# Optimization experiments

Hardware: AMD Instinct MI355X
Metric: run time of the kernel (lower is better)

## Reference

```python
import jax, jax.numpy as jnp
import numpy as np

B, S, D, H = 2, 2048, 1024, 16
DH = D // H
DIM_K = 1024


def setup_inputs() -> dict:
    key = jax.random.key(0)
    ks = jax.random.split(key, 5)
    sc = 0.02
    return {
        "x": jax.random.normal(ks[0], (B, S, D), dtype=jnp.float32),
        "Wq": jax.random.normal(ks[1], (D, DIM_K), dtype=jnp.float32) * sc,
        "Wk": jax.random.normal(ks[2], (D, DIM_K), dtype=jnp.float32) * sc,
        "Wv": jax.random.normal(ks[3], (D, DIM_K), dtype=jnp.float32) * sc,
        "Wo": jax.random.normal(ks[4], (DIM_K, DIM_K), dtype=jnp.float32) * sc,
    }


def reference(x, Wq, Wk, Wv, Wo):
    # projections (Linear, no bias); weights stored as [in, out]
    q = (x @ Wq).reshape(B, S, H, DH).transpose(0, 2, 1, 3)  # [B,H,S,DH]
    k = (x @ Wk).reshape(B, S, H, DH).transpose(0, 2, 1, 3)
    v = (x @ Wv).reshape(B, S, H, DH).transpose(0, 2, 1, 3)

    scores = jnp.einsum("bhqd,bhkd->bhqk", q, k)  # [B,H,S,S]
    # causal mask applied BEFORE scaling, as in the original
    causal_mask = jnp.triu(jnp.ones((S, S), dtype=bool), k=1)
    m_inf = -jnp.finfo(scores.dtype).max
    scores = jnp.where(causal_mask[None, None], m_inf, scores)
    attn = jax.nn.softmax(scores * (DIM_K ** -0.5), axis=-1)

    out = jnp.einsum("bhqk,bhkd->bhqd", attn, v)  # [B,H,S,DH]
    out = out.transpose(0, 2, 1, 3).reshape(B, S, DIM_K)
    return out @ Wo
```

## Files before the change

### kernel.cpp

```cpp
#include <hip/hip_runtime.h>


#define AS1 __attribute__((address_space(1)))
#define AS3 __attribute__((address_space(3)))
#define EXPC2 0.04508422f
#define C24 1.08202128f

typedef __attribute__((ext_vector_type(4))) float f32x4;
typedef __attribute__((ext_vector_type(8))) short bf16x8;

__device__ __forceinline__ void gload16(const void* g, void* l) {
  __builtin_amdgcn_global_load_lds((const AS1 unsigned int*)g,
                                   (AS3 unsigned int*)l, 16, 0, 0);
}
__device__ __forceinline__ unsigned short f2b(float f) {
  unsigned u = __float_as_uint(f);
  return (unsigned short)((u + 0x7FFFu + ((u >> 16) & 1u)) >> 16);
}
__device__ __forceinline__ float fexp2(float x) {
  float r;
  asm("v_exp_f32 %0, %1" : "=v"(r) : "v"(x));
  return r;
}
__device__ __forceinline__ unsigned cvtpk(float a, float b) {
  unsigned r;
  asm("v_cvt_pk_bf16_f32 %0, %1, %2" : "=v"(r) : "v"(a), "v"(b));
  return r;
}

__global__ __launch_bounds__(256) void prep(
    const float* __restrict__ x, const float* __restrict__ W0,
    const float* __restrict__ W1, const float* __restrict__ W2,
    const float* __restrict__ W3, unsigned short* __restrict__ xb,
    unsigned short* __restrict__ Wt) {
  __shared__ float T[64][65];
  const int tid = threadIdx.x;
  const int bid = blockIdx.x;
  if (bid < 4096) {
    const size_t i = (size_t)(bid * 256 + tid) * 4;
    float4 v = *(const float4*)&x[i];
    uint2 o;
    o.x = f2b(v.x) | ((unsigned)f2b(v.y) << 16);
    o.y = f2b(v.z) | ((unsigned)f2b(v.w) << 16);
    *(uint2*)&xb[i] = o;
    return;
  }
  const int idx = bid - 4096;
  const int kb = (idx & 15) * 64, nb = ((idx >> 4) & 15) * 64, z = idx >> 8;
  const float* W = (z == 0) ? W0 : (z == 1) ? W1 : (z == 2) ? W2 : W3;
  unsigned short* D = Wt + (size_t)z * 1024 * 1024;
#pragma unroll
  for (int p = 0; p < 4; ++p) {
    const int s = p * 256 + tid;
    const int r = s >> 4, c4 = s & 15;
    float4 v = *(const float4*)&W[(size_t)(kb + r) * 1024 + nb + c4 * 4];
    T[r][c4 * 4 + 0] = v.x;
    T[r][c4 * 4 + 1] = v.y;
    T[r][c4 * 4 + 2] = v.z;
    T[r][c4 * 4 + 3] = v.w;
  }
  __syncthreads();
#pragma unroll
  for (int p = 0; p < 4; ++p) {
    const int s = p * 256 + tid;
    const int n = s >> 4, k4 = s & 15;
    uint2 o;
    o.x = f2b(T[k4 * 4 + 0][n]) | ((unsigned)f2b(T[k4 * 4 + 1][n]) << 16);
    o.y = f2b(T[k4 * 4 + 2][n]) | ((unsigned)f2b(T[k4 * 4 + 3][n]) << 16);
    *(uint2*)&D[(size_t)(nb + n) * 1024 + kb + k4 * 4] = o;
  }
}

__global__ __launch_bounds__(512, 2) void gemm_qkv(
    const unsigned short* __restrict__ xb, const unsigned short* __restrict__ Wt,
    unsigned short* __restrict__ Qb, unsigned short* __restrict__ Kb,
    unsigned short* __restrict__ Vp) {
  __shared__ unsigned short smem[65536];

  const int tid = threadIdx.x, lane = tid & 63, w = tid >> 6;
  const int bm = blockIdx.x & 15, bn = blockIdx.x >> 4;
  const int wr = w >> 2, wc = w & 3;

  f32x4 acc[8][4];
#pragma unroll
  for (int m = 0; m < 8; ++m)
#pragma unroll
    for (int n = 0; n < 4; ++n) acc[m][n] = (f32x4)0.0f;

  const int prow0 = tid >> 3, pc0 = tid & 7;
  const int u0 = pc0 ^ (prow0 & 7);
  const int aRow0 = bm * 256 + 2 * prow0 + (u0 >> 2);
  const int bRow0 = bn * 256 + 2 * prow0 + (u0 >> 2);
  const int cOff = (u0 & 3) * 8;

  const int fr = lane & 15, g = lane >> 4;
  const int frh = fr >> 1;
  const int pcx = ((((fr & 1) << 2) | g) ^ frh) * 8;

#define STAGE8(BUF, KS, KC)                                                   \
  {                                                                           \
    const size_t ko = (size_t)(KC) + (KS)*32 + cOff;                          \
    gload16(&xb[(size_t)aRow0 * 1024 + ko],                                   \
            &smem[(BUF)*32768 + (KS)*8192 + tid * 8]);                        \
    gload16(&xb[(size_t)(aRow0 + 128) * 1024 + ko],                           \
            &smem[(BUF)*32768 + (KS)*8192 + 4096 + tid * 8]);                 \
    gload16(&Wt[(size_t)bRow0 * 1024 + ko],                                   \
            &smem[(BUF)*32768 + 16384 + (KS)*8192 + tid * 8]);                \
    gload16(&Wt[(size_t)(bRow0 + 128) * 1024 + ko],                           \
            &smem[(BUF)*32768 + 16384 + (KS)*8192 + 4096 + tid * 8]);         \
  }

#define PHASE(CUR, KS, VMSTR, STAGESTMT)                                      \
  {                                                                           \
    asm volatile(VMSTR ::: "memory");                                         \
    __builtin_amdgcn_sched_barrier(0);                                        \
    __builtin_amdgcn_s_barrier();                                             \
    __builtin_amdgcn_sched_barrier(0);                                        \
    bf16x8 af[8], bf[4];                                                      \
    const unsigned short* Ab_ = &smem[(CUR)*32768 + (KS)*8192];               \
    const unsigned short* Bb_ = &smem[(CUR)*32768 + 16384 + (KS)*8192];       \
    _Pragma("unroll") for (int mf = 0; mf < 8; ++mf) af[mf] =                 \
        *(const bf16x8*)&Ab_[(wr * 64 + mf * 8 + frh) * 64 + pcx];            \
    _Pragma("unroll") for (int nf = 0; nf < 4; ++nf) bf[nf] =                 \
        *(const bf16x8*)&Bb_[(wc * 32 + nf * 8 + frh) * 64 + pcx];            \
    STAGESTMT;                                                                \
    __builtin_amdgcn_s_setprio(1);                                            \
    _Pragma("unroll") for (int mf = 0; mf < 8; ++mf)                          \
        _Pragma("unroll") for (int nf = 0; nf < 4; ++nf) acc[mf][nf] =        \
            __builtin_amdgcn_mfma_f32_16x16x32_bf16(af[mf], bf[nf],           \
                                                    acc[mf][nf], 0, 0, 0);    \
    __builtin_amdgcn_s_setprio(0);                                            \
  }

  STAGE8(0, 0, 0)
  STAGE8(0, 1, 0)

#pragma unroll 1
  for (int t = 0; t < 15; ++t) {
    const int cu_ = t & 1, nb_ = (t + 1) & 1;
    const int kc1 = (t + 1) * 64;
    PHASE(cu_, 0, "s_waitcnt vmcnt(4)", STAGE8(nb_, 0, kc1))
    PHASE(cu_, 1, "s_waitcnt vmcnt(4)", STAGE8(nb_, 1, kc1))
  }
  PHASE(1, 0, "s_waitcnt vmcnt(4)", (void)0)
  PHASE(1, 1, "s_waitcnt vmcnt(0)", (void)0)

  if (bn < 8) {
    unsigned short* Ob = (bn < 4) ? Qb : Kb;
    const int cbase = (bn & 3) * 256;
#pragma unroll
    for (int mf = 0; mf < 8; ++mf)
#pragma unroll
      for (int nf = 0; nf < 4; ++nf) {
        const int col = cbase + wc * 64 + nf * 16 + fr;
        const int h = col >> 6, d = col & 63;
#pragma unroll
        for (int rr = 0; rr < 4; ++rr) {
          const int m = bm * 256 + wr * 128 + mf * 16 + g * 4 + rr;
          const int b = m >> 11, s = m & 2047;
          Ob[((size_t)(b * 16 + h) * 2048 + s) * 64 + d] = f2b(acc[mf][nf][rr]);
        }
      }
    return;
  }

  const int chb = (bn - 8) * 256;
  const int s0all = bm * 256;
  const int b = s0all >> 11;
#pragma unroll
  for (int qq = 0; qq < 4; ++qq) {
    const int qm = qq >> 1, qn = qq & 1;
    __syncthreads();
    if (wr == qm && (wc >> 1) == qn) {
#pragma unroll
      for (int mf = 0; mf < 8; ++mf)
#pragma unroll
        for (int nf = 0; nf < 4; ++nf) {
          const int cl = (wc & 1) * 64 + nf * 16 + fr;
#pragma unroll
          for (int rr = 0; rr < 4; ++rr) {
            const int ml = mf * 16 + g * 4 + rr;
            const int u = ml & 63, a = u >> 4;
            const int sperm = (ml & 64) | ((a >> 1) * 32 + ((u >> 2) & 3) * 8 +
                                           (a & 1) * 4 + (u & 3));
            smem[cl * 132 + sperm] = f2b(acc[mf][nf][rr]);
          }
        }
    }
    __syncthreads();
    const int row = tid >> 2, cg = (tid & 3) * 32;
    const int ch = chb + qn * 128 + row;
    const int h = ch >> 6, d = ch & 63;
    const int sb = (s0all + qm * 128) & 2047;
    unsigned short* dst = &Vp[((size_t)(b * 16 + h) * 64 + d) * 2048 + sb + cg];
    *(uint4*)(dst + 0) = *(const uint4*)&smem[row * 132 + cg];
    *(uint4*)(dst + 8) = *(const uint4*)&smem[row * 132 + cg + 8];
    *(uint4*)(dst + 16) = *(const uint4*)&smem[row * 132 + cg + 16];
    *(uint4*)(dst + 24) = *(const uint4*)&smem[row * 132 + cg + 24];
  }
#undef PHASE
#undef STAGE8
}

__global__ __launch_bounds__(256) void gemm_out(
    const unsigned short* __restrict__ A, const unsigned short* __restrict__ B,
    float* __restrict__ Of) {
  __shared__ unsigned short smem[32768];

  const int tid = threadIdx.x, lane = tid & 63, w = tid >> 6;
  const int bm = blockIdx.x >> 3, bn = blockIdx.x & 7;
  const int wr = w >> 1, wc = w & 1;

  f32x4 acc[4][4];
#pragma unroll
  for (int m = 0; m < 4; ++m)
#pragma unroll
    for (int n = 0; n < 4; ++n) acc[m][n] = (f32x4)0.0f;

  const int prow0 = tid >> 3, pc0 = tid & 7;
  const int u0 = pc0 ^ (prow0 & 7);
  const int rOff = 2 * prow0 + (u0 >> 2);
  const int cOff = (u0 & 3) * 8;

  const int fr = lane & 15, g = lane >> 4;
  const int frh = fr >> 1;
  const int pcx = ((((fr & 1) << 2) | g) ^ frh) * 8;

#define OSTAGE4(BUF, KS, KC)                                                  \
  {                                                                           \
    const size_t ko = (size_t)(KC) + (KS)*32 + cOff;                          \
    gload16(&A[(size_t)(bm * 128 + rOff) * 1024 + ko],                        \
            &smem[(BUF)*16384 + (KS)*4096 + tid * 8]);                        \
    gload16(&A[(size_t)(bm * 128 + 64 + rOff) * 1024 + ko],                   \
            &smem[(BUF)*16384 + (KS)*4096 + 2048 + tid * 8]);                 \
    gload16(&B[(size_t)(bn * 128 + rOff) * 1024 + ko],                        \
            &smem[(BUF)*16384 + 8192 + (KS)*4096 + tid * 8]);                 \
    gload16(&B[(size_t)(bn * 128 + 64 + rOff) * 1024 + ko],                   \
            &smem[(BUF)*16384 + 8192 + (KS)*4096 + 2048 + tid * 8]);          \
  }

#define OPHASE(CUR, KS, VMSTR, STAGESTMT)                                     \
  {                                                                           \
    asm volatile(VMSTR ::: "memory");                                         \
    __builtin_amdgcn_sched_barrier(0);                                        \
    __builtin_amdgcn_s_barrier();                                             \
    __builtin_amdgcn_sched_barrier(0);                                        \
    bf16x8 af[4], bf[4];                                                      \
    const unsigned short* Ab_ = &smem[(CUR)*16384 + (KS)*4096];               \
    const unsigned short* Bb_ = &smem[(CUR)*16384 + 8192 + (KS)*4096];        \
    _Pragma("unroll") for (int mf = 0; mf < 4; ++mf) af[mf] =                 \
        *(const bf16x8*)&Ab_[(wr * 32 + mf * 8 + frh) * 64 + pcx];            \
    _Pragma("unroll") for (int nf = 0; nf < 4; ++nf) bf[nf] =                 \
        *(const bf16x8*)&Bb_[(wc * 32 + nf * 8 + frh) * 64 + pcx];            \
    STAGESTMT;                                                                \
    __builtin_amdgcn_s_setprio(1);                                            \
    _Pragma("unroll") for (int mf = 0; mf < 4; ++mf)                          \
        _Pragma("unroll") for (int nf = 0; nf < 4; ++nf) acc[mf][nf] =        \
            __builtin_amdgcn_mfma_f32_16x16x32_bf16(af[mf], bf[nf],           \
                                                    acc[mf][nf], 0, 0, 0);    \
    __builtin_amdgcn_s_setprio(0);                                            \
  }

  OSTAGE4(0, 0, 0)
  OSTAGE4(0, 1, 0)

#pragma unroll 1
  for (int t = 0; t < 15; ++t) {
    const int cu_ = t & 1, nb_ = (t + 1) & 1;
    const int kc1 = (t + 1) * 64;
    OPHASE(cu_, 0, "s_waitcnt vmcnt(4)", OSTAGE4(nb_, 0, kc1))
    OPHASE(cu_, 1, "s_waitcnt vmcnt(4)", OSTAGE4(nb_, 1, kc1))
  }
  OPHASE(1, 0, "s_waitcnt vmcnt(4)", (void)0)
  OPHASE(1, 1, "s_waitcnt vmcnt(0)", (void)0)

#pragma unroll
  for (int mf = 0; mf < 4; ++mf)
#pragma unroll
    for (int nf = 0; nf < 4; ++nf) {
      const int col = bn * 128 + wc * 64 + nf * 16 + fr;
#pragma unroll
      for (int rr = 0; rr < 4; ++rr) {
        const int m = bm * 128 + wr * 64 + mf * 16 + g * 4 + rr;
        Of[(size_t)m * 1024 + col] = acc[mf][nf][rr];
      }
    }
#undef OPHASE
#undef OSTAGE4
}

__global__ __launch_bounds__(256) void attn_fm(
    const unsigned short* __restrict__ Qb, const unsigned short* __restrict__ Kb,
    const unsigned short* __restrict__ Vp, unsigned short* __restrict__ Ab) {
  __shared__ unsigned short smem[16384];

  const int tid = threadIdx.x, lane = tid & 63, w = tid >> 6;
  const int lo = lane & 15, hi = lane >> 4;

  const int id = blockIdx.x;
  const int qtr = id >> 8;
  const int g = (id >> 5) & 7;
  const int bh = id & 31;
  const int bq = (qtr == 0)   ? 2 * g
                 : (qtr == 1) ? 2 * g + 1
                 : (qtr == 2) ? 31 - 2 * g
                              : 30 - 2 * g;
  const int qw = bq * 64 + w * 16;
  const size_t base = (size_t)bh * (2048 * 64);

  bf16x8 qf[2];
#pragma unroll
  for (int ks = 0; ks < 2; ++ks)
    qf[ks] =
        *(const bf16x8*)&Qb[base + (size_t)(qw + lo) * 64 + ks * 32 + hi * 8];

  f32x4 accO[4];
#pragma unroll
  for (int mf = 0; mf < 4; ++mf) accO[mf] = (f32x4)0.0f;
  float lpart = 0.0f;

  const int ntile = bq + 1;
  const unsigned short* kgb = Kb + base;
  const unsigned short* vgb = Vp + base;
  const int lseg = w * 512;

#define STAGE(BUF, KBASE)                                                    \
  {                                                                          \
    const int kb_ = (KBASE);                                                 \
    _Pragma("unroll") for (int qq = 0; qq < 2; ++qq) {                       \
      const int slot = qq * 256 + tid;                                       \
      const int row = slot >> 3, ch = (slot & 7) ^ (row & 7);                \
      gload16(kgb + (size_t)(kb_ + row) * 64 + ch * 8,                       \
              &smem[(BUF)*4096 + qq * 2048 + lseg]);                         \
      gload16(vgb + (size_t)row * 2048 + kb_ + ch * 8,                       \
              &smem[8192 + (BUF)*4096 + qq * 2048 + lseg]);                  \
    }                                                                        \
  }

  STAGE(0, 0)
  int cur = 0;

  for (int t = 0; t < ntile; ++t) {
    __syncthreads();
    if (t + 1 < ntile) STAGE(cur ^ 1, (t + 1) * 64)

    const int kb = t * 64;
    const int x7 = lo & 7;
    bf16x8 ka[2][4];
#pragma unroll
    for (int ks = 0; ks < 2; ++ks) {
      const int ch = (ks * 4 + hi) ^ x7;
#pragma unroll
      for (int kf = 0; kf < 4; ++kf)
        ka[ks][kf] =
            *(const bf16x8*)&smem[cur * 4096 + (kf * 16 + lo) * 64 + ch * 8];
    }
    f32x4 st[4];
#pragma unroll
    for (int kf = 0; kf < 4; ++kf) st[kf] = (f32x4)0.0f;
    __builtin_amdgcn_s_setprio(1);
#pragma unroll
    for (int ks = 0; ks < 2; ++ks)
#pragma unroll
      for (int kf = 0; kf < 4; ++kf)
        st[kf] = __builtin_amdgcn_mfma_f32_16x16x32_bf16(ka[ks][kf], qf[ks],
                                                         st[kf], 0, 0, 0);
    __builtin_amdgcn_s_setprio(0);

    bf16x8 va[2][4];
#pragma unroll
    for (int ks = 0; ks < 2; ++ks) {
      const int ch = (ks * 4 + hi) ^ x7;
#pragma unroll
      for (int mf = 0; mf < 4; ++mf)
        va[ks][mf] = *(const bf16x8*)&smem[8192 + cur * 4096 +
                                           (mf * 16 + lo) * 64 + ch * 8];
    }

    float v[16];
#pragma unroll
    for (int kf = 0; kf < 4; ++kf)
#pragma unroll
      for (int rr = 0; rr < 4; ++rr) v[kf * 4 + rr] = st[kf][rr];
    if (kb + 63 > qw) {
      const int qg = qw + lo;
#pragma unroll
      for (int kf = 0; kf < 4; ++kf)
#pragma unroll
        for (int rr = 0; rr < 4; ++rr)
          if (kb + kf * 16 + hi * 4 + rr > qg) v[kf * 4 + rr] = -1e30f;
    }
    float p[16], rs = 0.0f;
#pragma unroll
    for (int i = 0; i < 16; ++i) {
      p[i] = fexp2(fmaf(v[i], EXPC2, -C24));
      rs += p[i];
    }
    lpart += rs;

    bf16x8 pb[2];
#pragma unroll
    for (int ks = 0; ks < 2; ++ks) {
      uint4 u;
      u.x = cvtpk(p[ks * 8 + 0], p[ks * 8 + 1]);
      u.y = cvtpk(p[ks * 8 + 2], p[ks * 8 + 3]);
      u.z = cvtpk(p[ks * 8 + 4], p[ks * 8 + 5]);
      u.w = cvtpk(p[ks * 8 + 6], p[ks * 8 + 7]);
      pb[ks] = *(bf16x8*)&u;
    }

    __builtin_amdgcn_s_setprio(1);
#pragma unroll
    for (int ks = 0; ks < 2; ++ks)
#pragma unroll
      for (int mf = 0; mf < 4; ++mf)
        accO[mf] = __builtin_amdgcn_mfma_f32_16x16x32_bf16(va[ks][mf], pb[ks],
                                                           accO[mf], 0, 0, 0);
    __builtin_amdgcn_s_setprio(0);
    cur ^= 1;
  }

  __syncthreads();

  float l = lpart;
  l += __shfl_xor(l, 16);
  l += __shfl_xor(l, 32);
  const float linv = 1.0f / l;
  unsigned short* ot = &smem[w * 1152];
#pragma unroll
  for (int mf = 0; mf < 4; ++mf) {
    uint2 u;
    u.x = cvtpk(accO[mf][0] * linv, accO[mf][1] * linv);
    u.y = cvtpk(accO[mf][2] * linv, accO[mf][3] * linv);
    *(uint2*)&ot[lo * 72 + mf * 16 + hi * 4] = u;
  }
  const int b = bh >> 4, h = bh & 15;
  const int row = lane >> 2, cg = (lane & 3) * 16;
  uint4 o0 = *(const uint4*)&ot[row * 72 + cg];
  uint4 o1 = *(const uint4*)&ot[row * 72 + cg + 8];
  unsigned short* op = &Ab[(size_t)(b * 2048 + qw + row) * 1024 + h * 64 + cg];
  *(uint4*)op = o0;
  *(uint4*)(op + 8) = o1;
#undef STAGE
}

extern "C" void kernel_launch(void* const* d_in, const int* in_sizes, int n_in,
                              void* d_out, int out_size, void* d_ws,
                              size_t ws_size, hipStream_t stream) {
  (void)in_sizes; (void)n_in; (void)out_size; (void)ws_size;
  const float* x = (const float*)d_in[0];
  const float* Wq = (const float*)d_in[1];
  const float* Wk = (const float*)d_in[2];
  const float* Wv = (const float*)d_in[3];
  const float* Wo = (const float*)d_in[4];
  float* out = (float*)d_out;

  char* ws = (char*)d_ws;
  unsigned short* xb = (unsigned short*)(ws);
  unsigned short* Wt = (unsigned short*)(ws + (8u << 20));
  unsigned short* Qb = (unsigned short*)(ws + (16u << 20));
  unsigned short* Kb = (unsigned short*)(ws + (24u << 20));
  unsigned short* Vp = (unsigned short*)(ws + (32u << 20));
  unsigned short* Ab = (unsigned short*)(ws + (40u << 20));
  unsigned short* Wto = Wt + (size_t)3 * 1024 * 1024;

  prep<<<dim3(5120), 256, 0, stream>>>(x, Wq, Wk, Wv, Wo, xb, Wt);
  gemm_qkv<<<dim3(192), 512, 0, stream>>>(xb, Wt, Qb, Kb, Vp);
  attn_fm<<<dim3(1024), 256, 0, stream>>>(Qb, Kb, Vp, Ab);
  gemm_out<<<dim3(256), 256, 0, stream>>>(Ab, Wto, out);
}
```

Before: 94.44 us.

## Pair causal query blocks per workgroup with triple-buffered K/V pipeline

The attention kernel now gives each workgroup two query blocks, p and 31-p, so every workgroup processes a fixed 33 key tiles. This balances the causal workload and halves the grid to 512 blocks. K/V staging moves from double to triple buffering, with explicit vmcnt waits and raw s_barrier phases that separate the K and V loads. LDS use rises to about 58KB per block, which may reduce occupancy, and the fixed vmcnt counts depend on exactly how the loads are issued.

```diff
diff --git a/kernel.cpp b/kernel.cpp
--- a/kernel.cpp
+++ b/kernel.cpp
@@ -289,159 +289,179 @@
 #undef OSTAGE4
 }
 
-__global__ __launch_bounds__(256) void attn_fm(
+__global__ __launch_bounds__(256) void attn_pipe(
     const unsigned short* __restrict__ Qb, const unsigned short* __restrict__ Kb,
     const unsigned short* __restrict__ Vp, unsigned short* __restrict__ Ab) {
-  __shared__ unsigned short smem[16384];
+  __shared__ unsigned short smem[29184];
 
   const int tid = threadIdx.x, lane = tid & 63, w = tid >> 6;
   const int lo = lane & 15, hi = lane >> 4;
+  const int x7 = lo & 7;
 
   const int id = blockIdx.x;
-  const int qtr = id >> 8;
-  const int g = (id >> 5) & 7;
   const int bh = id & 31;
-  const int bq = (qtr == 0)   ? 2 * g
-                 : (qtr == 1) ? 2 * g + 1
-                 : (qtr == 2) ? 31 - 2 * g
-                              : 30 - 2 * g;
-  const int qw = bq * 64 + w * 16;
+  const int p = id >> 5;
+  const int qw0 = p * 64 + w * 16;
+  const int qw1 = (31 - p) * 64 + w * 16;
   const size_t base = (size_t)bh * (2048 * 64);
-
-  bf16x8 qf[2];
-#pragma unroll
-  for (int ks = 0; ks < 2; ++ks)
-    qf[ks] =
-        *(const bf16x8*)&Qb[base + (size_t)(qw + lo) * 64 + ks * 32 + hi * 8];
-
-  f32x4 accO[4];
-#pragma unroll
-  for (int mf = 0; mf < 4; ++mf) accO[mf] = (f32x4)0.0f;
-  float lpart = 0.0f;
-
-  const int ntile = bq + 1;
   const unsigned short* kgb = Kb + base;
   const unsigned short* vgb = Vp + base;
   const int lseg = w * 512;
-
-#define STAGE(BUF, KBASE)                                                    \
+  const int b = bh >> 4, h = bh & 15;
+
+  auto kbof = [&](int s) { return (s <= p ? s : s - p - 1) * 64; };
+
+  bf16x8 qA0, qA1, qB0, qB1;
+  qA0 = *(const bf16x8*)&Qb[base + (size_t)(qw0 + lo) * 64 + 0 * 32 + hi * 8];
+  qA1 = *(const bf16x8*)&Qb[base + (size_t)(qw0 + lo) * 64 + 1 * 32 + hi * 8];
+  qB0 = *(const bf16x8*)&Qb[base + (size_t)(qw1 + lo) * 64 + 0 * 32 + hi * 8];
+  qB1 = *(const bf16x8*)&Qb[base + (size_t)(qw1 + lo) * 64 + 1 * 32 + hi * 8];
+  bf16x8 qc0 = qA0, qc1 = qA1;
+
+  f32x4 accO[4];
+#pragma unroll
+  for (int mf = 0; mf < 4; ++mf) accO[mf] = (f32x4)0.0f;
+  float lpart = 0.0f;
+  int qwc = qw0;
+
+  const int srow = tid >> 3;
+  const int sch = ((tid & 7) ^ (srow & 7)) * 8;
+
+#define AST(BUF, KB_)                                                        \
   {                                                                          \
-    const int kb_ = (KBASE);                                                 \
-    _Pragma("unroll") for (int qq = 0; qq < 2; ++qq) {                       \
-      const int slot = qq * 256 + tid;                                       \
-      const int row = slot >> 3, ch = (slot & 7) ^ (row & 7);                \
-      gload16(kgb + (size_t)(kb_ + row) * 64 + ch * 8,                       \
-              &smem[(BUF)*4096 + qq * 2048 + lseg]);                         \
-      gload16(vgb + (size_t)row * 2048 + kb_ + ch * 8,                       \
-              &smem[8192 + (BUF)*4096 + qq * 2048 + lseg]);                  \
+    const int kb_ = (KB_);                                                   \
+    gload16(kgb + (size_t)(kb_ + srow) * 64 + sch, &smem[(BUF)*4096 + lseg]); \
+    gload16(kgb + (size_t)(kb_ + 32 + srow) * 64 + sch,                      \
+            &smem[(BUF)*4096 + 2048 + lseg]);                                \
+    __builtin_amdgcn_sched_barrier(0);                                       \
+    gload16(vgb + (size_t)srow * 2048 + kb_ + sch,                           \
+            &smem[12288 + (BUF)*4096 + lseg]);                               \
+    gload16(vgb + (size_t)(32 + srow) * 2048 + kb_ + sch,                    \
+            &smem[12288 + (BUF)*4096 + 2048 + lseg]);                        \
+    __builtin_amdgcn_sched_barrier(0);                                       \
+  }
+
+#define KPHASE(CB, VMSTR)                                                    \
+  asm volatile(VMSTR ::: "memory");                                          \
+  __builtin_amdgcn_sched_barrier(0);                                         \
+  __builtin_amdgcn_s_barrier();                                              \
+  __builtin_amdgcn_sched_barrier(0);                                         \
+  bf16x8 ka[2][4];                                                           \
+  _Pragma("unroll") for (int ks = 0; ks < 2; ++ks) {                         \
+    const int ch = (ks * 4 + hi) ^ x7;                                       \
+    _Pragma("unroll") for (int kf = 0; kf < 4; ++kf) ka[ks][kf] =            \
+        *(const bf16x8*)&smem[(CB)*4096 + (kf * 16 + lo) * 64 + ch * 8];     \
+  }                                                                          \
+  f32x4 st[4];                                                               \
+  _Pragma("unroll") for (int kf = 0; kf < 4; ++kf) st[kf] = (f32x4)0.0f;     \
+  __builtin_amdgcn_s_setprio(1);                                             \
+  _Pragma("unroll") for (int ks = 0; ks < 2; ++ks) {                         \
+    _Pragma("unroll") for (int kf = 0; kf < 4; ++kf) st[kf] =                \
+        __builtin_amdgcn_mfma_f32_16x16x32_bf16(                             \
+            ka[ks][kf], (ks == 0) ? qc0 : qc1, st[kf], 0, 0, 0);             \
+  }                                                                          \
+  __builtin_amdgcn_s_setprio(0);
+
+#define VPHASE(CB, VMSTR, STAGESTMT, KBV)                                    \
+  asm volatile(VMSTR ::: "memory");                                          \
+  __builtin_amdgcn_sched_barrier(0);                                         \
+  __builtin_amdgcn_s_barrier();                                              \
+  __builtin_amdgcn_sched_barrier(0);                                         \
+  bf16x8 va[2][4];                                                           \
+  _Pragma("unroll") for (int ks = 0; ks < 2; ++ks) {                         \
+    const int ch = (ks * 4 + hi) ^ x7;                                       \
+    _Pragma("unroll") for (int mf = 0; mf < 4; ++mf) va[ks][mf] =            \
+        *(const bf16x8*)&smem[12288 + (CB)*4096 + (mf * 16 + lo) * 64 +      \
+                              ch * 8];                                       \
+  }                                                                          \
+  STAGESTMT;                                                                 \
+  float v[16];                                                               \
+  _Pragma("unroll") for (int kf = 0; kf < 4; ++kf)                           \
+      _Pragma("unroll") for (int rr = 0; rr < 4; ++rr) v[kf * 4 + rr] =      \
+          st[kf][rr];                                                        \
+  if ((KBV) + 63 > qwc) {                                                    \
+    const int qg = qwc + lo;                                                 \
+    _Pragma("unroll") for (int kf = 0; kf < 4; ++kf)                         \
+        _Pragma("unroll") for (int rr = 0; rr < 4; ++rr) if ((KBV) +         \
+            kf * 16 + hi * 4 + rr > qg) v[kf * 4 + rr] = -1e30f;             \
+  }                                                                          \
+  float pe[16], rs = 0.0f;                                                   \
+  _Pragma("unroll") for (int i = 0; i < 16; ++i) {                           \
+    pe[i] = fexp2(fmaf(v[i], EXPC2, -C24));                                  \
+    rs += pe[i];                                                             \
+  }                                                                          \
+  lpart += rs;                                                               \
+  bf16x8 pb[2];                                                              \
+  _Pragma("unroll") for (int ks = 0; ks < 2; ++ks) {                         \
+    uint4 u;                                                                 \
+    u.x = cvtpk(pe[ks * 8 + 0], pe[ks * 8 + 1]);                             \
+    u.y = cvtpk(pe[ks * 8 + 2], pe[ks * 8 + 3]);                             \
+    u.z = cvtpk(pe[ks * 8 + 4], pe[ks * 8 + 5]);                             \
+    u.w = cvtpk(pe[ks * 8 + 6], pe[ks * 8 + 7]);                             \
+    pb[ks] = *(bf16x8*)&u;                                                   \
+  }                                                                          \
+  __builtin_amdgcn_s_setprio(1);                                             \
+  _Pragma("unroll") for (int ks = 0; ks < 2; ++ks)                           \
+      _Pragma("unroll") for (int mf = 0; mf < 4; ++mf) accO[mf] =            \
+          __builtin_amdgcn_mfma_f32_16x16x32_bf16(va[ks][mf], pb[ks],        \
+                                                  accO[mf], 0, 0, 0);        \
+  __builtin_amdgcn_s_setprio(0);
+
+#define EPI(QW)                                                              \
+  {                                                                          \
+    float l = lpart;                                                         \
+    l += __shfl_xor(l, 16);                                                  \
+    l += __shfl_xor(l, 32);                                                  \
+    const float linv = 1.0f / l;                                             \
+    unsigned short* ot = &smem[24576 + w * 1152];                            \
+    _Pragma("unroll") for (int mf = 0; mf < 4; ++mf) {                       \
+      uint2 u;                                                               \
+      u.x = cvtpk(accO[mf][0] * linv, accO[mf][1] * linv);                   \
+      u.y = cvtpk(accO[mf][2] * linv, accO[mf][3] * linv);                   \
+      *(uint2*)&ot[lo * 72 + mf * 16 + hi * 4] = u;                          \
     }                                                                        \
-  }
-
-  STAGE(0, 0)
-  int cur = 0;
-
-  for (int t = 0; t < ntile; ++t) {
-    __syncthreads();
-    if (t + 1 < ntile) STAGE(cur ^ 1, (t + 1) * 64)
-
-    const int kb = t * 64;
-    const int x7 = lo & 7;
-    bf16x8 ka[2][4];
-#pragma unroll
-    for (int ks = 0; ks < 2; ++ks) {
-      const int ch = (ks * 4 + hi) ^ x7;
-#pragma unroll
-      for (int kf = 0; kf < 4; ++kf)
-        ka[ks][kf] =
-            *(const bf16x8*)&smem[cur * 4096 + (kf * 16 + lo) * 64 + ch * 8];
+    const int row_ = lane >> 2, cg_ = (lane & 3) * 16;                       \
+    uint4 o0 = *(const uint4*)&ot[row_ * 72 + cg_];                          \
+    uint4 o1 = *(const uint4*)&ot[row_ * 72 + cg_ + 8];                      \
+    unsigned short* op =                                                     \
+        &Ab[(size_t)(b * 2048 + (QW) + row_) * 1024 + h * 64 + cg_];         \
+    *(uint4*)op = o0;                                                        \
+    *(uint4*)(op + 8) = o1;                                                  \
+  }
+
+  AST(0, 0)
+  AST(1, kbof(1))
+
+#pragma unroll 1
+  for (int c = 0; c < 32; ++c) {
+    const int cb = c % 3;
+    const int kb = kbof(c);
+    {
+      KPHASE(cb, "s_waitcnt vmcnt(6)")
+      VPHASE(cb, "s_waitcnt vmcnt(4)",
+             if (c < 31) AST((c + 2) % 3, kbof(c + 2)), kb)
     }
-    f32x4 st[4];
-#pragma unroll
-    for (int kf = 0; kf < 4; ++kf) st[kf] = (f32x4)0.0f;
-    __builtin_amdgcn_s_setprio(1);
-#pragma unroll
-    for (int ks = 0; ks < 2; ++ks)
-#pragma unroll
-      for (int kf = 0; kf < 4; ++kf)
-        st[kf] = __builtin_amdgcn_mfma_f32_16x16x32_bf16(ka[ks][kf], qf[ks],
-                                                         st[kf], 0, 0, 0);
-    __builtin_amdgcn_s_setprio(0);
-
-    bf16x8 va[2][4];
-#pragma unroll
-    for (int ks = 0; ks < 2; ++ks) {
-      const int ch = (ks * 4 + hi) ^ x7;
-#pragma unroll
-      for (int mf = 0; mf < 4; ++mf)
-        va[ks][mf] = *(const bf16x8*)&smem[8192 + cur * 4096 +
-                                           (mf * 16 + lo) * 64 + ch * 8];
+    if (c == p) {
+      EPI(qw0)
+#pragma unroll
+      for (int mf = 0; mf < 4; ++mf) accO[mf] = (f32x4)0.0f;
+      lpart = 0.0f;
+      qc0 = qB0;
+      qc1 = qB1;
+      qwc = qw1;
     }
-
-    float v[16];
-#pragma unroll
-    for (int kf = 0; kf < 4; ++kf)
-#pragma unroll
-      for (int rr = 0; rr < 4; ++rr) v[kf * 4 + rr] = st[kf][rr];
-    if (kb + 63 > qw) {
-      const int qg = qw + lo;
-#pragma unroll
-      for (int kf = 0; kf < 4; ++kf)
-#pragma unroll
-        for (int rr = 0; rr < 4; ++rr)
-          if (kb + kf * 16 + hi * 4 + rr > qg) v[kf * 4 + rr] = -1e30f;
-    }
-    float p[16], rs = 0.0f;
-#pragma unroll
-    for (int i = 0; i < 16; ++i) {
-      p[i] = fexp2(fmaf(v[i], EXPC2, -C24));
-      rs += p[i];
-    }
-    lpart += rs;
-
-    bf16x8 pb[2];
-#pragma unroll
-    for (int ks = 0; ks < 2; ++ks) {
-      uint4 u;
-      u.x = cvtpk(p[ks * 8 + 0], p[ks * 8 + 1]);
-      u.y = cvtpk(p[ks * 8 + 2], p[ks * 8 + 3]);
-      u.z = cvtpk(p[ks * 8 + 4], p[ks * 8 + 5]);
-      u.w = cvtpk(p[ks * 8 + 6], p[ks * 8 + 7]);
-      pb[ks] = *(bf16x8*)&u;
-    }
-
-    __builtin_amdgcn_s_setprio(1);
-#pragma unroll
-    for (int ks = 0; ks < 2; ++ks)
-#pragma unroll
-      for (int mf = 0; mf < 4; ++mf)
-        accO[mf] = __builtin_amdgcn_mfma_f32_16x16x32_bf16(va[ks][mf], pb[ks],
-                                                           accO[mf], 0, 0, 0);
-    __builtin_amdgcn_s_setprio(0);
-    cur ^= 1;
-  }
-
-  __syncthreads();
-
-  float l = lpart;
-  l += __shfl_xor(l, 16);
-  l += __shfl_xor(l, 32);
-  const float linv = 1.0f / l;
-  unsigned short* ot = &smem[w * 1152];
-#pragma unroll
-  for (int mf = 0; mf < 4; ++mf) {
-    uint2 u;
-    u.x = cvtpk(accO[mf][0] * linv, accO[mf][1] * linv);
-    u.y = cvtpk(accO[mf][2] * linv, accO[mf][3] * linv);
-    *(uint2*)&ot[lo * 72 + mf * 16 + hi * 4] = u;
-  }
-  const int b = bh >> 4, h = bh & 15;
-  const int row = lane >> 2, cg = (lane & 3) * 16;
-  uint4 o0 = *(const uint4*)&ot[row * 72 + cg];
-  uint4 o1 = *(const uint4*)&ot[row * 72 + cg + 8];
-  unsigned short* op = &Ab[(size_t)(b * 2048 + qw + row) * 1024 + h * 64 + cg];
-  *(uint4*)op = o0;
-  *(uint4*)(op + 8) = o1;
-#undef STAGE
+  }
+  {
+    const int cb = 32 % 3;
+    const int kb = kbof(32);
+    KPHASE(cb, "s_waitcnt vmcnt(2)")
+    VPHASE(cb, "s_waitcnt vmcnt(0)", (void)0, kb)
+  }
+  EPI(qw1)
+#undef EPI
+#undef VPHASE
+#undef KPHASE
+#undef AST
 }
 
 extern "C" void kernel_launch(void* const* d_in, const int* in_sizes, int n_in,
@@ -466,6 +486,6 @@
 
   prep<<<dim3(5120), 256, 0, stream>>>(x, Wq, Wk, Wv, Wo, xb, Wt);
   gemm_qkv<<<dim3(192), 512, 0, stream>>>(xb, Wt, Qb, Kb, Vp);
-  attn_fm<<<dim3(1024), 256, 0, stream>>>(Qb, Kb, Vp, Ab);
+  attn_pipe<<<dim3(512), 256, 0, stream>>>(Qb, Kb, Vp, Ab);
   gemm_out<<<dim3(256), 256, 0, stream>>>(Ab, Wto, out);
 }
```

Result: slower. 96.42 us (+2.1%).
